# Optimization experiments

Measured on AMD Instinct MI355X. Metric: run time of the kernel, lower is better.

## Reference

```python
import jax, jax.numpy as jnp
import numpy as np

NUM_GROUPS = 32
EPS = 1e-5


def group_norm(x, gamma, beta):
    # x: [B, C, H, W]; normalize per group of C//NUM_GROUPS channels over (c_in_group, H, W)
    B, C, H, W = x.shape
    xg = x.reshape(B, NUM_GROUPS, C // NUM_GROUPS, H, W)
    mean = jnp.mean(xg, axis=(2, 3, 4), keepdims=True)
    var = jnp.var(xg, axis=(2, 3, 4), keepdims=True)
    xn = ((xg - mean) * jax.lax.rsqrt(var + EPS)).reshape(B, C, H, W)
    return xn * gamma[None, :, None, None] + beta[None, :, None, None]


def setup_inputs() -> dict:
    key = jax.random.key(0)
    kx, kq, kp = jax.random.split(key, 3)
    B, C, H, W = 4, 256, 64, 64
    x = jax.random.normal(kx, (B, C, H, W), dtype=jnp.float32)
    gamma = jnp.ones((C,), dtype=jnp.float32)
    beta = jnp.zeros((C,), dtype=jnp.float32)
    # 1x1 convs == channel matmuls; weights [out_c, in_c]
    w_qkv = jax.random.normal(kq, (3 * C, C), dtype=jnp.float32) / np.sqrt(C)
    w_proj = jax.random.normal(kp, (C, C), dtype=jnp.float32) / np.sqrt(C)
    return {"x": x, "t": 0, "gamma": gamma, "beta": beta, "w_qkv": w_qkv, "w_proj": w_proj}


def reference(x, t, gamma, beta, w_qkv, w_proj):
    B, C, H, W = x.shape
    normed = group_norm(x, gamma, beta)  # [B,C,H,W]
    qkv = jnp.einsum('bchw,oc->bohw', normed, w_qkv)  # [B,3C,H,W]
    q, k, v = jnp.split(qkv, 3, axis=1)
    N = H * W
    q = q.reshape(B, C, N)
    k = k.reshape(B, C, N)
    v = v.reshape(B, C, N)
    # scores[b,i,j] = sum_c q[b,c,i] k[b,c,j] / sqrt(C)
    scores = jnp.einsum('bci,bcj->bij', q, k) / jnp.sqrt(jnp.asarray(C, x.dtype))
    attn = jax.nn.softmax(scores, axis=-1)  # [B,N,N]
    # out[b,c,i] = sum_j v[b,c,j] attn[b,i,j]
    out = jnp.einsum('bcj,bij->bci', v, attn).reshape(B, C, H, W)
    out = jnp.einsum('bchw,oc->bohw', out, w_proj)
    return x + out
```

## Files before the change

kernel.cpp:

```cpp
#include <hip/hip_runtime.h>

typedef __bf16 bf16x8 __attribute__((ext_vector_type(8)));
typedef float floatx4 __attribute__((ext_vector_type(4)));
typedef float floatx16 __attribute__((ext_vector_type(16)));
typedef unsigned int u32;

#define BB 4
#define CC 256
#define NN 4096

__device__ __forceinline__ unsigned short f2bf(float f) {
  union { float f; unsigned u; } v; v.f = f;
  unsigned r = v.u + 0x7fffu + ((v.u >> 16) & 1u);
  return (unsigned short)(r >> 16);
}

__device__ __forceinline__ float bf2f(unsigned short s) {
  union { unsigned u; float f; } v; v.u = ((u32)s) << 16;
  return v.f;
}

__device__ __forceinline__ void async16(const void* g, void* l) {
  __builtin_amdgcn_global_load_lds((const __attribute__((address_space(1))) u32*)g,
                                   (__attribute__((address_space(3))) u32*)l, 16, 0, 0);
}

__device__ __forceinline__ u32 fbits(float f) {
  union { float f; u32 u; } v; v.f = f; return v.u;
}

__global__ __launch_bounds__(256) void gn_stats(const float* __restrict__ x, float* __restrict__ mr) {
  int bg = blockIdx.x;
  const float* p = x + (size_t)bg * 32768;
  int t = threadIdx.x;
  float s = 0.f, q = 0.f;
#pragma unroll
  for (int it = 0; it < 32; ++it) {
    float4 v = *(const float4*)(p + it * 1024 + t * 4);
    s += v.x + v.y + v.z + v.w;
    q += v.x * v.x + v.y * v.y + v.z * v.z + v.w * v.w;
  }
#pragma unroll
  for (int off = 1; off < 64; off <<= 1) {
    s += __shfl_xor(s, off, 64);
    q += __shfl_xor(q, off, 64);
  }
  __shared__ float red[8];
  int w = t >> 6;
  if ((t & 63) == 0) { red[w] = s; red[4 + w] = q; }
  __syncthreads();
  if (t == 0) {
    float S = red[0] + red[1] + red[2] + red[3];
    float Q = red[4] + red[5] + red[6] + red[7];
    float mean = S * (1.f / 32768.f);
    float var = Q * (1.f / 32768.f) - mean * mean;
    mr[bg] = mean;
    mr[128 + bg] = rsqrtf(var + 1e-5f);
  }
}

__global__ __launch_bounds__(256) void gn_apply(const float* __restrict__ x, const float* __restrict__ mr,
                                                const float* __restrict__ gamma, const float* __restrict__ beta,
                                                unsigned short* __restrict__ normed) {
  int bid = blockIdx.x;
  int nt = bid & 63;
  int ct = (bid >> 6) & 3;
  int b = bid >> 8;
  int c0 = ct * 64, n0 = nt * 64;
  __shared__ unsigned short T[64][80];
  int t = threadIdx.x;
#pragma unroll
  for (int it = 0; it < 4; ++it) {
    int idx = it * 256 + t;
    int cl = idx >> 4;
    int n4 = (idx & 15) * 4;
    int c = c0 + cl;
    int bg = b * 32 + (c >> 3);
    float mean = mr[bg], rstd = mr[128 + bg];
    float sc = rstd * gamma[c];
    float sh = beta[c] - mean * sc;
    float4 v = *(const float4*)(x + ((size_t)(b * CC + c)) * NN + n0 + n4);
    T[n4 + 0][cl] = f2bf(v.x * sc + sh);
    T[n4 + 1][cl] = f2bf(v.y * sc + sh);
    T[n4 + 2][cl] = f2bf(v.z * sc + sh);
    T[n4 + 3][cl] = f2bf(v.w * sc + sh);
  }
  __syncthreads();
#pragma unroll
  for (int it = 0; it < 2; ++it) {
    int idx = it * 256 + t;
    int nl = idx >> 3, ck = idx & 7;
    uint4 val;
    unsigned short* pv = (unsigned short*)&val;
#pragma unroll
    for (int j = 0; j < 8; ++j) pv[j] = T[nl][ck * 8 + j];
    *(uint4*)(normed + ((size_t)b * NN + n0 + nl) * CC + c0 + ck * 8) = val;
  }
}

__global__ __launch_bounds__(256) void wconv(const float* __restrict__ wqkv, const float* __restrict__ wproj,
                                             unsigned short* __restrict__ wq_bf, unsigned short* __restrict__ wp_bf) {
  int i = blockIdx.x * 256 + threadIdx.x;
  if (i < 196608) {
    float v = wqkv[i];
    if (i < 65536) v *= 0.090168440055560213f;
    wq_bf[i] = f2bf(v);
  } else {
    int j = i - 196608;
    wp_bf[j] = f2bf(wproj[j]);
  }
}

template <int RESID>
__global__ __launch_bounds__(256) void gemm_bt(const unsigned short* __restrict__ A,
                                               const unsigned short* __restrict__ Bm,
                                               void* __restrict__ Cout, const float* __restrict__ resid,
                                               int mtiles, int ldc,
                                               long sA, long sB, long sC, long sR) {
  int mt = blockIdx.x % mtiles;
  int nt = blockIdx.x / mtiles;
  int b = blockIdx.y;
  int m0 = mt * 128, n0 = nt * 128;
  __shared__ unsigned short As[128][72];
  __shared__ unsigned short Bs[128][72];
  int t = threadIdx.x;
  int w = t >> 6, lane = t & 63;
  int l16 = lane & 15, quad = lane >> 4;
  int wr = w >> 1, wc = w & 1;
  const unsigned short* Ab = A + (size_t)b * sA + (size_t)m0 * 256;
  const unsigned short* Bb = Bm + (size_t)b * sB + (size_t)n0 * 256;
  floatx4 acc[4][4];
#pragma unroll
  for (int m = 0; m < 4; ++m)
#pragma unroll
    for (int n = 0; n < 4; ++n)
#pragma unroll
      for (int r = 0; r < 4; ++r) acc[m][n][r] = 0.f;

  for (int kb = 0; kb < 4; ++kb) {
    __syncthreads();
#pragma unroll
    for (int i = 0; i < 4; ++i) {
      int idx = i * 256 + t;
      int r = idx >> 3, ck = idx & 7;
      *(uint4*)&As[r][ck * 8] = *(const uint4*)(Ab + (size_t)r * 256 + kb * 64 + ck * 8);
      *(uint4*)&Bs[r][ck * 8] = *(const uint4*)(Bb + (size_t)r * 256 + kb * 64 + ck * 8);
    }
    __syncthreads();
#pragma unroll
    for (int kk = 0; kk < 2; ++kk) {
      bf16x8 af[4], bfr[4];
#pragma unroll
      for (int m = 0; m < 4; ++m) af[m] = *(const bf16x8*)&As[wr * 64 + m * 16 + l16][kk * 32 + quad * 8];
#pragma unroll
      for (int n = 0; n < 4; ++n) bfr[n] = *(const bf16x8*)&Bs[wc * 64 + n * 16 + l16][kk * 32 + quad * 8];
#pragma unroll
      for (int m = 0; m < 4; ++m)
#pragma unroll
        for (int n = 0; n < 4; ++n)
          acc[m][n] = __builtin_amdgcn_mfma_f32_16x16x32_bf16(af[m], bfr[n], acc[m][n], 0, 0, 0);
    }
  }
  size_t cb = (size_t)b * sC;
  size_t rb = (size_t)b * sR;
#pragma unroll
  for (int m = 0; m < 4; ++m)
#pragma unroll
    for (int n = 0; n < 4; ++n)
#pragma unroll
      for (int r = 0; r < 4; ++r) {
        int row = m0 + wr * 64 + m * 16 + quad * 4 + r;
        int col = n0 + wc * 64 + n * 16 + l16;
        size_t idx = (size_t)row * ldc + col;
        if (RESID)
          ((float*)Cout)[cb + idx] = acc[m][n][r] + resid[rb + idx];
        else
          ((unsigned short*)Cout)[cb + idx] = f2bf(acc[m][n][r]);
      }
}

__global__ __launch_bounds__(512, 2) void attn(const unsigned short* __restrict__ qk,
                                               const unsigned short* __restrict__ vbuf,
                                               unsigned short* __restrict__ opart0,
                                               unsigned short* __restrict__ opart1,
                                               float* __restrict__ lpart) {
  __shared__ __attribute__((aligned(16))) char smem[131072];

  int xcd = blockIdx.x & 7, slot = blockIdx.x >> 3;
  int b = xcd >> 1;
  int kh = xcd & 1;
  int i0 = slot * 128;
  int k0 = kh * 32;

  int t = threadIdx.x, w = t >> 6, l = t & 63;
  int l31 = l & 31, hi = l >> 5;
  int jh = w & 1;
  int iq = w >> 1;

  const size_t bqk = (size_t)b * NN * 512;
  const size_t bv = (size_t)b * CC * NN;

  auto stage = [&](int tile, int buf) {
    const unsigned short* kg = qk + bqk + (size_t)tile * 64 * 512 + 256;
    char* kb = smem + buf * 32768;
#pragma unroll
    for (int it = 0; it < 4; ++it) {
      int pp = w * 4 + it;
      int r = 2 * pp + (l >> 5);
      int c = (l & 31) ^ (r & 31);
      async16(kg + (size_t)r * 512 + c * 8, kb + pp * 1024);
    }
    const unsigned short* vg = vbuf + bv + (size_t)tile * 64;
    char* vb = smem + 65536 + buf * 32768;
    int cj = (l & 7) ^ ((l >> 3) & 7);
#pragma unroll
    for (int it = 0; it < 4; ++it) {
      int pp = w * 4 + it;
      int rc = 8 * pp + (l >> 3);
      async16(vg + (size_t)rc * NN + cj * 8, vb + pp * 1024);
    }
  };

  stage(k0, 0);

  bf16x8 qreg[16];
  {
    const unsigned short* qp = qk + bqk + (size_t)(i0 + iq * 32 + l31) * 512 + hi * 8;
#pragma unroll
    for (int ks = 0; ks < 16; ++ks)
      qreg[ks] = *(const bf16x8*)(qp + ks * 16);
  }

  floatx16 oacc[8];
#pragma unroll
  for (int cf = 0; cf < 8; ++cf)
#pragma unroll
    for (int r = 0; r < 16; ++r) oacc[cf][r] = 0.f;
  float lacc = 0.f;

  for (int kt = 0; kt < 32; ++kt) {
    int cur = kt & 1;
    __syncthreads();
    if (kt < 31) stage(k0 + kt + 1, cur ^ 1);

    const unsigned short* Kc = (const unsigned short*)(smem + cur * 32768);
    const unsigned short* Vc = (const unsigned short*)(smem + 65536 + cur * 32768);

    floatx16 st;
#pragma unroll
    for (int r = 0; r < 16; ++r) st[r] = 0.f;
#pragma unroll
    for (int ks = 0; ks < 16; ++ks) {
      bf16x8 kf = *(const bf16x8*)&Kc[(jh * 32 + l31) * 256 + (((ks << 1) | hi) ^ l31) * 8];
      st = __builtin_amdgcn_mfma_f32_32x32x16_bf16(kf, qreg[ks], st, 0, 0, 0);
    }

    u32 pr[8];
#pragma unroll
    for (int k2 = 0; k2 < 8; ++k2) {
      float p0 = __builtin_amdgcn_exp2f(st[2 * k2]);
      float p1 = __builtin_amdgcn_exp2f(st[2 * k2 + 1]);
      lacc += p0 + p1;
      pr[k2] = __builtin_amdgcn_perm(fbits(p1), fbits(p0), 0x07060302u);
    }

    union U { u32 u[4]; bf16x8 v; } a0, a1;
    {
      u32 sA = hi ? pr[0] : pr[2], sB = hi ? pr[1] : pr[3];
      u32 rA = (u32)__shfl_xor((int)sA, 32, 64);
      u32 rB = (u32)__shfl_xor((int)sB, 32, 64);
      a0.u[0] = hi ? rA : pr[0]; a0.u[1] = hi ? rB : pr[1];
      a0.u[2] = hi ? pr[2] : rA; a0.u[3] = hi ? pr[3] : rB;
      sA = hi ? pr[4] : pr[6]; sB = hi ? pr[5] : pr[7];
      rA = (u32)__shfl_xor((int)sA, 32, 64);
      rB = (u32)__shfl_xor((int)sB, 32, 64);
      a1.u[0] = hi ? rA : pr[4]; a1.u[1] = hi ? rB : pr[5];
      a1.u[2] = hi ? pr[6] : rA; a1.u[3] = hi ? pr[7] : rB;
    }

#pragma unroll
    for (int cf = 0; cf < 8; ++cf) {
      const unsigned short* vrow = Vc + (cf * 32 + l31) * 64;
      bf16x8 v0 = *(const bf16x8*)(vrow + (((jh * 4) | hi) ^ (l31 & 7)) * 8);
      oacc[cf] = __builtin_amdgcn_mfma_f32_32x32x16_bf16(a0.v, v0, oacc[cf], 0, 0, 0);
      bf16x8 v1 = *(const bf16x8*)(vrow + (((jh * 4 + 2) | hi) ^ (l31 & 7)) * 8);
      oacc[cf] = __builtin_amdgcn_mfma_f32_32x32x16_bf16(a1.v, v1, oacc[cf], 0, 0, 0);
    }
  }

  float l2 = lacc + __shfl_xor(lacc, 32, 64);

  float* Of = (float*)smem + iq * 8192;
  __syncthreads();
  if (jh == 1) {
#pragma unroll
    for (int cf = 0; cf < 8; ++cf)
#pragma unroll
      for (int r = 0; r < 16; ++r) {
        int il = (r & 3) + 8 * (r >> 2) + 4 * hi;
        Of[il * 256 + cf * 32 + l31] = oacc[cf][r];
      }
  }
  __syncthreads();
  unsigned short* ops = kh ? opart1 : opart0;
  size_t rowbase = (size_t)b * NN + i0 + iq * 32;
  if (jh == 0) {
#pragma unroll
    for (int cf = 0; cf < 8; ++cf)
#pragma unroll
      for (int r = 0; r < 16; ++r) {
        int il = (r & 3) + 8 * (r >> 2) + 4 * hi;
        float v = oacc[cf][r] + Of[il * 256 + cf * 32 + l31];
        ops[(rowbase + il) * CC + cf * 32 + l31] = f2bf(v);
      }
  }
  __syncthreads();
  float* Lred = (float*)smem;
  if (hi == 0) Lred[w * 32 + l31] = l2;
  __syncthreads();
  if (jh == 0 && hi == 0) {
    size_t pbl = (size_t)(b * 2 + kh) * NN + i0;
    lpart[pbl + iq * 32 + l31] = Lred[(iq * 2) * 32 + l31] + Lred[(iq * 2 + 1) * 32 + l31];
  }
}

__global__ __launch_bounds__(256) void gemm_proj(const unsigned short* __restrict__ wp,
                                                 const unsigned short* __restrict__ op0,
                                                 const unsigned short* __restrict__ op1,
                                                 const float* __restrict__ lp,
                                                 float* __restrict__ out, const float* __restrict__ x) {
  int mt = blockIdx.x & 1;
  int nt = blockIdx.x >> 1;
  int b = blockIdx.y;
  int m0 = mt * 128, n0 = nt * 128;
  __shared__ unsigned short As[128][72];
  __shared__ unsigned short Bs[128][72];
  __shared__ float Linv[128];
  int t = threadIdx.x;
  int w = t >> 6, lane = t & 63;
  int l16 = lane & 15, quad = lane >> 4;
  int wr = w >> 1, wc = w & 1;
  const unsigned short* Ab = wp + (size_t)m0 * 256;
  const unsigned short* o0 = op0 + ((size_t)b * NN + n0) * 256;
  const unsigned short* o1 = op1 + ((size_t)b * NN + n0) * 256;
  if (t < 128) Linv[t] = 1.f / (lp[b * 8192 + n0 + t] + lp[b * 8192 + 4096 + n0 + t]);
  floatx4 acc[4][4];
#pragma unroll
  for (int m = 0; m < 4; ++m)
#pragma unroll
    for (int n = 0; n < 4; ++n)
#pragma unroll
      for (int r = 0; r < 4; ++r) acc[m][n][r] = 0.f;

  for (int kb = 0; kb < 4; ++kb) {
    __syncthreads();
#pragma unroll
    for (int i = 0; i < 4; ++i) {
      int idx = i * 256 + t;
      int r = idx >> 3, ck = idx & 7;
      *(uint4*)&As[r][ck * 8] = *(const uint4*)(Ab + (size_t)r * 256 + kb * 64 + ck * 8);
      uint4 u0 = *(const uint4*)(o0 + (size_t)r * 256 + kb * 64 + ck * 8);
      uint4 u1 = *(const uint4*)(o1 + (size_t)r * 256 + kb * 64 + ck * 8);
      float li = Linv[r];
      const unsigned short* pa = (const unsigned short*)&u0;
      const unsigned short* pb = (const unsigned short*)&u1;
      union { unsigned short us[8]; uint4 q; } ob;
#pragma unroll
      for (int j = 0; j < 8; ++j)
        ob.us[j] = f2bf((bf2f(pa[j]) + bf2f(pb[j])) * li);
      *(uint4*)&Bs[r][ck * 8] = ob.q;
    }
    __syncthreads();
#pragma unroll
    for (int kk = 0; kk < 2; ++kk) {
      bf16x8 af[4], bfr[4];
#pragma unroll
      for (int m = 0; m < 4; ++m) af[m] = *(const bf16x8*)&As[wr * 64 + m * 16 + l16][kk * 32 + quad * 8];
#pragma unroll
      for (int n = 0; n < 4; ++n) bfr[n] = *(const bf16x8*)&Bs[wc * 64 + n * 16 + l16][kk * 32 + quad * 8];
#pragma unroll
      for (int m = 0; m < 4; ++m)
#pragma unroll
        for (int n = 0; n < 4; ++n)
          acc[m][n] = __builtin_amdgcn_mfma_f32_16x16x32_bf16(af[m], bfr[n], acc[m][n], 0, 0, 0);
    }
  }
  size_t cb = (size_t)b * CC * NN;
#pragma unroll
  for (int m = 0; m < 4; ++m)
#pragma unroll
    for (int n = 0; n < 4; ++n)
#pragma unroll
      for (int r = 0; r < 4; ++r) {
        int row = m0 + wr * 64 + m * 16 + quad * 4 + r;
        int col = n0 + wc * 64 + n * 16 + l16;
        size_t idx = cb + (size_t)row * NN + col;
        out[idx] = acc[m][n][r] + x[idx];
      }
}

extern "C" void kernel_launch(void* const* d_in, const int* in_sizes, int n_in,
                              void* d_out, int out_size, void* d_ws, size_t ws_size,
                              hipStream_t stream) {
  const float* x     = (const float*)d_in[0];
  const float* gamma = (const float*)d_in[2];
  const float* beta  = (const float*)d_in[3];
  const float* wqkv  = (const float*)d_in[4];
  const float* wproj = (const float*)d_in[5];
  float* out = (float*)d_out;

  char* p = (char*)d_ws;
  float* mr               = (float*)(p + 0);
  unsigned short* wq_bf   = (unsigned short*)(p + 1024);
  unsigned short* wp_bf   = (unsigned short*)(p + 394240);
  unsigned short* normed  = (unsigned short*)(p + 525312);
  unsigned short* qkbuf   = (unsigned short*)(p + 8913920);
  unsigned short* vbuf    = (unsigned short*)(p + 25691136);
  unsigned short* opart1  = (unsigned short*)(p + 34079744);
  unsigned short* opart0  = normed;
  float* lpart            = (float*)(p + 1024);
  unsigned short* wv_bf   = wq_bf + 512 * 256;

  wconv<<<1024, 256, 0, stream>>>(wqkv, wproj, wq_bf, wp_bf);
  gn_stats<<<128, 256, 0, stream>>>(x, mr);
  gn_apply<<<1024, 256, 0, stream>>>(x, mr, gamma, beta, normed);
  gemm_bt<0><<<dim3(128, 4), 256, 0, stream>>>(normed, wq_bf, qkbuf, nullptr,
                                               32, 512, (long)NN * CC, 0L, (long)NN * 512, 0L);
  gemm_bt<0><<<dim3(64, 4), 256, 0, stream>>>(wv_bf, normed, vbuf, nullptr,
                                              2, 4096, 0L, (long)NN * CC, (long)CC * NN, 0L);
  attn<<<256, 512, 0, stream>>>(qkbuf, vbuf, opart0, opart1, lpart);
  gemm_proj<<<dim3(64, 4), 256, 0, stream>>>(wp_bf, opart0, opart1, lpart, out, x);
}
```

Before: 194.8 us.

## Double-buffer QKV/V GEMM loads with async global-to-LDS and XOR swizzle; fuse wconv into gn_stats

New measurement: 195.4 us. Within noise of the previous version (+0.3%).

```diff
diff --git a/kernel.cpp b/kernel.cpp
--- a/kernel.cpp
+++ b/kernel.cpp
@@ -29,8 +29,22 @@
   union { float f; u32 u; } v; v.f = f; return v.u;
 }
 
-__global__ __launch_bounds__(256) void gn_stats(const float* __restrict__ x, float* __restrict__ mr) {
-  int bg = blockIdx.x;
+__global__ __launch_bounds__(256) void gn_stats_wconv(const float* __restrict__ x, float* __restrict__ mr,
+                                                      const float* __restrict__ wqkv, const float* __restrict__ wproj,
+                                                      unsigned short* __restrict__ wq_bf, unsigned short* __restrict__ wp_bf) {
+  if (blockIdx.x < 1024) {
+    int i = blockIdx.x * 256 + threadIdx.x;
+    if (i < 196608) {
+      float v = wqkv[i];
+      if (i < 65536) v *= 0.090168440055560213f;
+      wq_bf[i] = f2bf(v);
+    } else {
+      int j = i - 196608;
+      wp_bf[j] = f2bf(wproj[j]);
+    }
+    return;
+  }
+  int bg = blockIdx.x - 1024;
   const float* p = x + (size_t)bg * 32768;
   int t = threadIdx.x;
   float s = 0.f, q = 0.f;
@@ -98,37 +112,37 @@
   }
 }
 
-__global__ __launch_bounds__(256) void wconv(const float* __restrict__ wqkv, const float* __restrict__ wproj,
-                                             unsigned short* __restrict__ wq_bf, unsigned short* __restrict__ wp_bf) {
-  int i = blockIdx.x * 256 + threadIdx.x;
-  if (i < 196608) {
-    float v = wqkv[i];
-    if (i < 65536) v *= 0.090168440055560213f;
-    wq_bf[i] = f2bf(v);
-  } else {
-    int j = i - 196608;
-    wp_bf[j] = f2bf(wproj[j]);
-  }
-}
-
 template <int RESID>
-__global__ __launch_bounds__(256) void gemm_bt(const unsigned short* __restrict__ A,
-                                               const unsigned short* __restrict__ Bm,
-                                               void* __restrict__ Cout, const float* __restrict__ resid,
-                                               int mtiles, int ldc,
-                                               long sA, long sB, long sC, long sR) {
+__global__ __launch_bounds__(256, 2) void gemm_bt2(const unsigned short* __restrict__ A,
+                                                   const unsigned short* __restrict__ Bm,
+                                                   void* __restrict__ Cout, const float* __restrict__ resid,
+                                                   int mtiles, int ldc,
+                                                   long sA, long sB, long sC, long sR) {
+  __shared__ __attribute__((aligned(16))) char smem[65536];
   int mt = blockIdx.x % mtiles;
   int nt = blockIdx.x / mtiles;
   int b = blockIdx.y;
   int m0 = mt * 128, n0 = nt * 128;
-  __shared__ unsigned short As[128][72];
-  __shared__ unsigned short Bs[128][72];
-  int t = threadIdx.x;
-  int w = t >> 6, lane = t & 63;
-  int l16 = lane & 15, quad = lane >> 4;
+  int t = threadIdx.x, w = t >> 6, l = t & 63;
+  int l16 = l & 15, quad = l >> 4;
   int wr = w >> 1, wc = w & 1;
   const unsigned short* Ab = A + (size_t)b * sA + (size_t)m0 * 256;
   const unsigned short* Bb = Bm + (size_t)b * sB + (size_t)n0 * 256;
+
+  auto stage = [&](int kb, int buf) {
+    int rsub = l >> 3;
+    int cj = (l & 7) ^ rsub;
+    char* ab = smem + buf * 16384;
+    char* bb = smem + 32768 + buf * 16384;
+#pragma unroll
+    for (int it = 0; it < 4; ++it) {
+      int pp = w * 4 + it;
+      size_t go = (size_t)(8 * pp + rsub) * 256 + kb * 64 + cj * 8;
+      async16(Ab + go, ab + pp * 1024);
+      async16(Bb + go, bb + pp * 1024);
+    }
+  };
+
   floatx4 acc[4][4];
 #pragma unroll
   for (int m = 0; m < 4; ++m)
@@ -137,23 +151,25 @@
 #pragma unroll
       for (int r = 0; r < 4; ++r) acc[m][n][r] = 0.f;
 
+  stage(0, 0);
+
+#pragma unroll 1
   for (int kb = 0; kb < 4; ++kb) {
+    int cur = kb & 1;
     __syncthreads();
-#pragma unroll
-    for (int i = 0; i < 4; ++i) {
-      int idx = i * 256 + t;
-      int r = idx >> 3, ck = idx & 7;
-      *(uint4*)&As[r][ck * 8] = *(const uint4*)(Ab + (size_t)r * 256 + kb * 64 + ck * 8);
-      *(uint4*)&Bs[r][ck * 8] = *(const uint4*)(Bb + (size_t)r * 256 + kb * 64 + ck * 8);
-    }
-    __syncthreads();
+    if (kb < 3) stage(kb + 1, cur ^ 1);
+    const unsigned short* As = (const unsigned short*)(smem + cur * 16384);
+    const unsigned short* Bs = (const unsigned short*)(smem + 32768 + cur * 16384);
 #pragma unroll
     for (int kk = 0; kk < 2; ++kk) {
       bf16x8 af[4], bfr[4];
-#pragma unroll
-      for (int m = 0; m < 4; ++m) af[m] = *(const bf16x8*)&As[wr * 64 + m * 16 + l16][kk * 32 + quad * 8];
-#pragma unroll
-      for (int n = 0; n < 4; ++n) bfr[n] = *(const bf16x8*)&Bs[wc * 64 + n * 16 + l16][kk * 32 + quad * 8];
+      int sw = ((kk * 4 + quad) ^ (l16 & 7)) * 8;
+#pragma unroll
+      for (int m = 0; m < 4; ++m)
+        af[m] = *(const bf16x8*)&As[(wr * 64 + m * 16 + l16) * 64 + sw];
+#pragma unroll
+      for (int n = 0; n < 4; ++n)
+        bfr[n] = *(const bf16x8*)&Bs[(wc * 64 + n * 16 + l16) * 64 + sw];
 #pragma unroll
       for (int m = 0; m < 4; ++m)
 #pragma unroll
@@ -161,6 +177,7 @@
           acc[m][n] = __builtin_amdgcn_mfma_f32_16x16x32_bf16(af[m], bfr[n], acc[m][n], 0, 0, 0);
     }
   }
+
   size_t cb = (size_t)b * sC;
   size_t rb = (size_t)b * sR;
 #pragma unroll
@@ -421,13 +438,12 @@
   float* lpart            = (float*)(p + 1024);
   unsigned short* wv_bf   = wq_bf + 512 * 256;
 
-  wconv<<<1024, 256, 0, stream>>>(wqkv, wproj, wq_bf, wp_bf);
-  gn_stats<<<128, 256, 0, stream>>>(x, mr);
+  gn_stats_wconv<<<1152, 256, 0, stream>>>(x, mr, wqkv, wproj, wq_bf, wp_bf);
   gn_apply<<<1024, 256, 0, stream>>>(x, mr, gamma, beta, normed);
-  gemm_bt<0><<<dim3(128, 4), 256, 0, stream>>>(normed, wq_bf, qkbuf, nullptr,
-                                               32, 512, (long)NN * CC, 0L, (long)NN * 512, 0L);
-  gemm_bt<0><<<dim3(64, 4), 256, 0, stream>>>(wv_bf, normed, vbuf, nullptr,
-                                              2, 4096, 0L, (long)NN * CC, (long)CC * NN, 0L);
+  gemm_bt2<0><<<dim3(128, 4), 256, 0, stream>>>(normed, wq_bf, qkbuf, nullptr,
+                                                32, 512, (long)NN * CC, 0L, (long)NN * 512, 0L);
+  gemm_bt2<0><<<dim3(64, 4), 256, 0, stream>>>(wv_bf, normed, vbuf, nullptr,
+                                               2, 4096, 0L, (long)NN * CC, (long)CC * NN, 0L);
   attn<<<256, 512, 0, stream>>>(qkbuf, vbuf, opart0, opart1, lpart);
   gemm_proj<<<dim3(64, 4), 256, 0, stream>>>(wp_bf, opart0, opart1, lpart, out, x);
 }
```
